# Performance work log

Measured on AMD Instinct MI355X. Metric: run time of the kernel, lower is better.

## Reference

```python
import jax, jax.numpy as jnp
import numpy as np
from jax import lax


def setup_inputs() -> dict:
    key = jax.random.key(0)
    k1, k2 = jax.random.split(key)
    B, T, C = 8, 4096, 256
    UNITS, WINDOW = 256, 2
    x = jax.random.normal(k1, (B, T, C), dtype=jnp.float32)
    kernel = jax.random.normal(k2, (WINDOW, C, 3 * UNITS), dtype=jnp.float32) * 0.05
    bias = jnp.zeros((3 * UNITS,), dtype=jnp.float32)
    return {"x": x, "kernel": kernel, "bias": bias}


def _qrnn_forward(x, kernel, bias):
    # Causal conv1d: left-pad time axis by (window - 1).
    window = kernel.shape[0]
    xp = jnp.pad(x, ((0, 0), (window - 1, 0), (0, 0)))
    gates = lax.conv_general_dilated(
        xp, kernel, window_strides=(1,), padding='VALID',
        dimension_numbers=('NWC', 'WIO', 'NWC')) + bias
    z, f, o = jnp.split(gates, 3, axis=-1)  # each [B, T, units]
    z = jnp.tanh(z)
    f = jax.nn.sigmoid(f)

    # fo_pool: c_t = f_t * c_{t-1} + (1 - f_t) * z_t, c_0 = 0.
    # Linear recurrence -> associative scan over time with elements (a, b):
    # compose((a1,b1),(a2,b2)) = (a1*a2, a2*b1 + b2).
    def combine(e1, e2):
        a1, b1 = e1
        a2, b2 = e2
        return a1 * a2, a2 * b1 + b2

    _, c = lax.associative_scan(combine, (f, (1.0 - f) * z), axis=1)
    h = jax.nn.sigmoid(o) * c  # output gate
    return h  # return_sequences=True -> [B, T, units]


def reference(x, kernel, bias):
    return _qrnn_forward(x, kernel, bias)
```

## Files before the change

### kernel.cpp

```cpp
#include <hip/hip_runtime.h>
#include <math.h>


#define Bq 8
#define Tq 4096
#define NCq 64
#define Lq 64

typedef __attribute__((ext_vector_type(8))) _Float16 f16x8;
typedef __attribute__((ext_vector_type(4))) float f32x4;

__device__ __forceinline__ float sigmoidf_(float x) {
    return 1.f / (1.f + __expf(-x));
}
__device__ __forceinline__ float tanh_fast(float x) {
    return 1.f - 2.f / (__expf(2.f * x) + 1.f);
}
__device__ __forceinline__ unsigned short f16b(float a) {
    _Float16 h = (_Float16)a;
    return *(unsigned short*)&h;
}
__device__ __forceinline__ void gload16(const void* g, void* l) {
    __builtin_amdgcn_global_load_lds(
        (const __attribute__((address_space(1))) void*)g,
        (__attribute__((address_space(3))) void*)l, 16, 0, 0);
}

__global__ __launch_bounds__(256) void split_x(
    const float* __restrict__ x, _Float16* __restrict__ xh)
{
    int idx = blockIdx.x * 256 + threadIdx.x;
    if (idx >= Bq * 4097 * 64) return;
    int b  = idx / (4097 * 64);
    int r  = idx % (4097 * 64);
    int tp = r / 64, c4 = (r % 64) << 2;
    size_t o = ((size_t)(b * 4097 + tp) << 8) + c4;
    _Float16 h4[4] = {(_Float16)0.f, (_Float16)0.f, (_Float16)0.f, (_Float16)0.f};
    if (tp > 0) {
        const float4 v = *(const float4*)&x[((size_t)(b * 4096 + tp - 1) << 8) + c4];
        h4[0] = (_Float16)v.x; h4[1] = (_Float16)v.y;
        h4[2] = (_Float16)v.z; h4[3] = (_Float16)v.w;
    }
    *(ushort4*)&xh[o] = *(ushort4*)h4;
}

__global__ __launch_bounds__(256) void split_k(
    const float* __restrict__ kw, _Float16* __restrict__ bh)
{
    int idx = blockIdx.x * 256 + threadIdx.x;
    if (idx >= 768 * 512) return;
    int n = idx >> 9, k = idx & 511;
    bh[((size_t)n << 9) + k] = (_Float16)kw[(size_t)k * 768 + n];
}

__global__ __launch_bounds__(256) void conv_gemm(
    const _Float16* __restrict__ xh, const _Float16* __restrict__ bth,
    const float* __restrict__ bias,
    _Float16* __restrict__ Z, _Float16* __restrict__ G, _Float16* __restrict__ SO)
{
    __shared__ __align__(16) char smem[32768];
    const int tid = threadIdx.x;
    const int l = tid & 63, w = tid >> 6;
    const int wr = w >> 1, wc = w & 1;
    const int bm = blockIdx.x;
    const int b  = bm >> 5;
    const int t0 = (bm & 31) << 7;
    const int n0 = blockIdx.y << 7;

    f32x4 acc[4][4] = {};

    const int rowT   = tid >> 2;
    const int slotSw = (tid & 3) ^ ((rowT >> 1) & 3);
    size_t gaBase = ((size_t)(b * 4097 + t0 + rowT) << 8) + (slotSw << 3);
    const int ldsW = w << 9;

    int offA[4];
    const int colB = (l >> 4) << 4;
    #pragma unroll
    for (int i = 0; i < 4; ++i) {
        int ra = wr * 64 + i * 16 + (l & 15);
        offA[i] = ((ra << 6) + colB) ^ (((ra >> 1) & 3) << 4);
    }
    size_t bB[4];
    #pragma unroll
    for (int ni = 0; ni < 4; ++ni)
        bB[ni] = ((size_t)(n0 + wc * 64 + ni * 16 + (l & 15)) << 9) + ((l >> 4) << 3);

    auto stageA = [&](int buf, int kk) {
        size_t ga = gaBase + (size_t)kk * 32;
        _Float16* pA = (_Float16*)smem + buf * 4096 + ldsW;
        gload16(xh + ga,         pA);
        gload16(xh + ga + 16384, pA + 2048);
    };
    auto loadB = [&](int kk, f16x8* fb) {
        #pragma unroll
        for (int ni = 0; ni < 4; ++ni)
            fb[ni] = *(const f16x8*)(bth + bB[ni] + (size_t)kk * 32);
    };
    auto computeA = [&](int buf, const f16x8* fb) {
        const char* bA = (const char*)smem + buf * 8192;
        f16x8 fa[4];
        #pragma unroll
        for (int i = 0; i < 4; ++i)
            fa[i] = *(const f16x8*)(bA + offA[i]);
        #pragma unroll
        for (int mi = 0; mi < 4; ++mi)
            #pragma unroll
            for (int ni = 0; ni < 4; ++ni)
                acc[mi][ni] = __builtin_amdgcn_mfma_f32_16x16x32_f16(
                    fa[mi], fb[ni], acc[mi][ni], 0, 0, 0);
    };

    f16x8 fbA[4], fbB[4];
    stageA(0, 0);
    loadB(0, fbA);
    __syncthreads();
    #pragma unroll
    for (int kp = 0; kp < 8; ++kp) {
        const int k0 = kp * 2;
        if (k0 + 1 < 16) { stageA(1, k0 + 1); loadB(k0 + 1, fbB); }
        computeA(0, fbA);
        if (k0 + 1 < 16) __syncthreads();
        if (k0 + 1 < 16) {
            if (k0 + 2 < 16) { stageA(0, k0 + 2); loadB(k0 + 2, fbA); }
            computeA(1, fbB);
            if (k0 + 2 < 16) __syncthreads();
        }
    }
    __syncthreads();

    const int gsel = (int)(blockIdx.y >> 1);
    float bb[4];
    #pragma unroll
    for (int ni = 0; ni < 4; ++ni)
        bb[ni] = bias[n0 + wc * 64 + ni * 16 + (l & 15)];

    unsigned short* Hd = (unsigned short*)smem;
    #pragma unroll
    for (int ni = 0; ni < 4; ++ni) {
        const int cl = wc * 64 + ni * 16 + (l & 15);
        #pragma unroll
        for (int mi = 0; mi < 4; ++mi)
            #pragma unroll
            for (int r = 0; r < 4; ++r) {
                const int trl = wr * 64 + mi * 16 + ((l >> 4) << 2) + r;
                float g = acc[mi][ni][r] + bb[ni];
                float a = (gsel == 0) ? tanh_fast(g)
                        : (gsel == 1) ? sigmoidf_(-g)
                                      : sigmoidf_(g);
                int byt = (trl << 8) + ((cl << 1) ^ (((trl >> 2) & 3) << 4));
                *(unsigned short*)((char*)Hd + byt) = f16b(a);
            }
    }
    __syncthreads();
    _Float16* Gg = (gsel == 0) ? Z : (gsel == 1) ? G : SO;
    const int u0 = n0 & 255;
    const size_t gbase = ((size_t)(b * 4096 + t0) << 8) + u0;
    #pragma unroll
    for (int j = 0; j < 8; ++j) {
        int hoff = tid * 8 + j * 2048;
        int row  = hoff >> 7;
        int cby  = (hoff & 127) << 1;
        int srcB = (row << 8) + (cby ^ (((row >> 2) & 3) << 4));
        int4 v = *(const int4*)((const char*)Hd + srcB);
        *(int4*)&Gg[gbase + ((size_t)row << 8) + (cby >> 1)] = v;
    }
}

__global__ __launch_bounds__(256) void chunk_reduce(
    const _Float16* __restrict__ Z, const _Float16* __restrict__ G,
    float* __restrict__ CA, float* __restrict__ CB)
{
    const int u = threadIdx.x;
    const int blk = blockIdx.x;
    const int b = blk >> 6, ck = blk & 63;
    size_t base = (((size_t)b << 12) + ck * Lq) * 256 + u;
    float A = 1.f, Bv = 0.f;
    #pragma unroll 8
    for (int s = 0; s < Lq; ++s) {
        size_t idx = base + (size_t)s * 256;
        float g = (float)G[idx];
        float z = (float)Z[idx];
        Bv = fmaf(1.f - g, Bv, g * z);
        A *= (1.f - g);
    }
    size_t cidx = ((size_t)b * NCq + ck) * 256 + u;
    CA[cidx] = A;
    CB[cidx] = Bv;
}

__global__ __launch_bounds__(256) void carry_scan(
    const float* __restrict__ CA, const float* __restrict__ CB,
    float* __restrict__ CIN)
{
    const int u = threadIdx.x;
    const int b = blockIdx.x;
    float c = 0.f;
    #pragma unroll 8
    for (int k = 0; k < NCq; ++k) {
        size_t idx = ((size_t)b * NCq + k) * 256 + u;
        CIN[idx] = c;
        c = fmaf(CA[idx], c, CB[idx]);
    }
}

__global__ __launch_bounds__(256) void apply_scan(
    const _Float16* __restrict__ Z, const _Float16* __restrict__ G,
    const _Float16* __restrict__ SO, const float* __restrict__ CIN,
    float* __restrict__ out)
{
    const int u = threadIdx.x;
    const int blk = blockIdx.x;
    const int b = blk >> 6, ck = blk & 63;
    float c = CIN[((size_t)b * NCq + ck) * 256 + u];
    size_t base = (((size_t)b << 12) + ck * Lq) * 256 + u;
    #pragma unroll 8
    for (int s = 0; s < Lq; ++s) {
        size_t idx = base + (size_t)s * 256;
        float g = (float)G[idx], z = (float)Z[idx];
        c = fmaf(1.f - g, c, g * z);
        out[idx] = (float)SO[idx] * c;
    }
}

extern "C" void kernel_launch(void* const* d_in, const int* in_sizes, int n_in,
                              void* d_out, int out_size, void* d_ws, size_t ws_size,
                              hipStream_t stream) {
    const float* x    = (const float*)d_in[0];
    const float* kw   = (const float*)d_in[1];
    const float* bias = (const float*)d_in[2];
    float* out = (float*)d_out;

    char* p = (char*)d_ws;
    _Float16* xh  = (_Float16*)p; p += (size_t)Bq * 4097 * 256 * 2;
    _Float16* bth = (_Float16*)p; p += (size_t)768 * 512 * 2;
    _Float16* Z   = (_Float16*)p; p += (size_t)Bq * Tq * 256 * 2;
    _Float16* G   = (_Float16*)p; p += (size_t)Bq * Tq * 256 * 2;
    _Float16* SO  = (_Float16*)p; p += (size_t)Bq * Tq * 256 * 2;
    float* CA  = (float*)p; p += (size_t)Bq * NCq * 256 * 4;
    float* CB  = (float*)p; p += (size_t)Bq * NCq * 256 * 4;
    float* CIN = (float*)p;

    split_x<<<(Bq * 4097 * 64 + 255) / 256, 256, 0, stream>>>(x, xh);
    split_k<<<(768 * 512 + 255) / 256, 256, 0, stream>>>(kw, bth);
    dim3 g1(256, 6);
    conv_gemm<<<g1, 256, 0, stream>>>(xh, bth, bias, Z, G, SO);
    chunk_reduce<<<512, 256, 0, stream>>>(Z, G, CA, CB);
    carry_scan<<<Bq, 256, 0, stream>>>(CA, CB, CIN);
    apply_scan<<<512, 256, 0, stream>>>(Z, G, SO, CIN, out);
}
```

Before: 106.2 us.

## Stage B tile through LDS with triple-buffered async loads and XCD-aware block remap

The conv GEMM now loads the weight tile into LDS with direct global-to-LDS loads, like the A tile, instead of having each wave read B fragments from global memory into registers. LDS grows to three 16KB stages, so loads run two k-steps ahead, gated by explicit vmcnt waits and raw barriers. The block index is also remapped so that consecutive blocks dispatched across the 8 XCDs share tiles for better L2 locality, and MFMA sections raise wave priority. The larger LDS footprint may lower occupancy, and the hand-tuned waitcnt values must match the number of loads issued per stage.

```diff
diff --git a/kernel.cpp b/kernel.cpp
--- a/kernel.cpp
+++ b/kernel.cpp
@@ -58,78 +58,85 @@
     const float* __restrict__ bias,
     _Float16* __restrict__ Z, _Float16* __restrict__ G, _Float16* __restrict__ SO)
 {
-    __shared__ __align__(16) char smem[32768];
+    __shared__ __align__(16) char smem[49152];
     const int tid = threadIdx.x;
     const int l = tid & 63, w = tid >> 6;
     const int wr = w >> 1, wc = w & 1;
-    const int bm = blockIdx.x;
+
+    const int p  = blockIdx.x + (blockIdx.y << 8);
+    const int Lw = (p & 7) * 192 + (p >> 3);
+    const int bm = Lw & 255;
+    const int by = Lw >> 8;
     const int b  = bm >> 5;
     const int t0 = (bm & 31) << 7;
-    const int n0 = blockIdx.y << 7;
+    const int n0 = by << 7;
 
     f32x4 acc[4][4] = {};
 
     const int rowT   = tid >> 2;
     const int slotSw = (tid & 3) ^ ((rowT >> 1) & 3);
     size_t gaBase = ((size_t)(b * 4097 + t0 + rowT) << 8) + (slotSw << 3);
+    size_t gbBase = ((size_t)(n0 + rowT) << 9) + (slotSw << 3);
     const int ldsW = w << 9;
 
-    int offA[4];
+    int offA[4], offB[4];
     const int colB = (l >> 4) << 4;
     #pragma unroll
     for (int i = 0; i < 4; ++i) {
         int ra = wr * 64 + i * 16 + (l & 15);
         offA[i] = ((ra << 6) + colB) ^ (((ra >> 1) & 3) << 4);
-    }
-    size_t bB[4];
-    #pragma unroll
-    for (int ni = 0; ni < 4; ++ni)
-        bB[ni] = ((size_t)(n0 + wc * 64 + ni * 16 + (l & 15)) << 9) + ((l >> 4) << 3);
-
-    auto stageA = [&](int buf, int kk) {
+        int rb = wc * 64 + i * 16 + (l & 15);
+        offB[i] = ((rb << 6) + colB) ^ (((rb >> 1) & 3) << 4);
+    }
+
+    auto stage = [&](int kk) {
+        const int buf = kk % 3;
+        _Float16* pA = (_Float16*)(smem + buf * 16384) + ldsW;
+        _Float16* pB = (_Float16*)(smem + buf * 16384 + 8192) + ldsW;
         size_t ga = gaBase + (size_t)kk * 32;
-        _Float16* pA = (_Float16*)smem + buf * 4096 + ldsW;
-        gload16(xh + ga,         pA);
-        gload16(xh + ga + 16384, pA + 2048);
+        size_t gb = gbBase + (size_t)kk * 32;
+        gload16(xh  + ga,          pA);
+        gload16(xh  + ga + 16384,  pA + 2048);
+        gload16(bth + gb,          pB);
+        gload16(bth + gb + 32768,  pB + 2048);
     };
-    auto loadB = [&](int kk, f16x8* fb) {
+
+    auto compute = [&](int kk) {
+        const char* bA = (const char*)smem + (kk % 3) * 16384;
+        const char* bB = bA + 8192;
+        f16x8 fa[4], fb[4];
         #pragma unroll
-        for (int ni = 0; ni < 4; ++ni)
-            fb[ni] = *(const f16x8*)(bth + bB[ni] + (size_t)kk * 32);
-    };
-    auto computeA = [&](int buf, const f16x8* fb) {
-        const char* bA = (const char*)smem + buf * 8192;
-        f16x8 fa[4];
-        #pragma unroll
-        for (int i = 0; i < 4; ++i)
+        for (int i = 0; i < 4; ++i) {
             fa[i] = *(const f16x8*)(bA + offA[i]);
+            fb[i] = *(const f16x8*)(bB + offB[i]);
+        }
+        __builtin_amdgcn_s_setprio(1);
         #pragma unroll
         for (int mi = 0; mi < 4; ++mi)
             #pragma unroll
             for (int ni = 0; ni < 4; ++ni)
                 acc[mi][ni] = __builtin_amdgcn_mfma_f32_16x16x32_f16(
                     fa[mi], fb[ni], acc[mi][ni], 0, 0, 0);
+        __builtin_amdgcn_s_setprio(0);
     };
 
-    f16x8 fbA[4], fbB[4];
-    stageA(0, 0);
-    loadB(0, fbA);
-    __syncthreads();
-    #pragma unroll
-    for (int kp = 0; kp < 8; ++kp) {
-        const int k0 = kp * 2;
-        if (k0 + 1 < 16) { stageA(1, k0 + 1); loadB(k0 + 1, fbB); }
-        computeA(0, fbA);
-        if (k0 + 1 < 16) __syncthreads();
-        if (k0 + 1 < 16) {
-            if (k0 + 2 < 16) { stageA(0, k0 + 2); loadB(k0 + 2, fbA); }
-            computeA(1, fbB);
-            if (k0 + 2 < 16) __syncthreads();
-        }
-    }
-    __syncthreads();
-
-    const int gsel = (int)(blockIdx.y >> 1);
+    stage(0);
+    stage(1);
+#define QSTEP(k, V) \
+    if ((k) + 2 < 16) stage((k) + 2); \
+    asm volatile("s_waitcnt vmcnt(" #V ")" ::: "memory"); \
+    __builtin_amdgcn_s_barrier(); \
+    compute(k); \
+    asm volatile("s_waitcnt lgkmcnt(0)" ::: "memory"); \
+    __builtin_amdgcn_sched_barrier(0); \
+    __builtin_amdgcn_s_barrier();
+    QSTEP(0, 8)  QSTEP(1, 8)  QSTEP(2, 8)  QSTEP(3, 8)
+    QSTEP(4, 8)  QSTEP(5, 8)  QSTEP(6, 8)  QSTEP(7, 8)
+    QSTEP(8, 8)  QSTEP(9, 8)  QSTEP(10, 8) QSTEP(11, 8)
+    QSTEP(12, 8) QSTEP(13, 8) QSTEP(14, 4) QSTEP(15, 0)
+#undef QSTEP
+
+    const int gsel = by >> 1;
     float bb[4];
     #pragma unroll
     for (int ni = 0; ni < 4; ++ni)
```

Measured after the change: 87.03 us. -18.0%, faster.

## Rewrite conv GEMM with 256x256 tiles, LDS-staged B, and explicit barrier pipeline

Applied to the files above, without the earlier changes.

The conv GEMM moves from 128x128 tiles with 4 waves to 256x256 tiles with 8 waves. Both A and B are now staged into a double-buffered 128KB LDS region through direct global-to-LDS loads with XOR swizzling. The K loop is fully unrolled into an explicit schedule that interleaves LDS fragment loads, async stages, raw s_barrier/vmcnt waits and setprio-raised MFMA bursts. The intent is more operand reuse and hiding of load latency behind MFMA. The cost is a large LDS footprint that limits occupancy, fewer blocks (384) for the machine, and higher register pressure from the 8x4 accumulator array.

```diff
diff --git a/kernel.cpp b/kernel.cpp
--- a/kernel.cpp
+++ b/kernel.cpp
@@ -53,116 +53,166 @@
     bh[((size_t)n << 9) + k] = (_Float16)kw[(size_t)k * 768 + n];
 }
 
-__global__ __launch_bounds__(256) void conv_gemm(
+__global__ __launch_bounds__(512, 2) void conv_gemm(
     const _Float16* __restrict__ xh, const _Float16* __restrict__ bth,
     const float* __restrict__ bias,
     _Float16* __restrict__ Z, _Float16* __restrict__ G, _Float16* __restrict__ SO)
 {
-    __shared__ __align__(16) char smem[32768];
+    __shared__ __align__(16) char smem[131072];
     const int tid = threadIdx.x;
     const int l = tid & 63, w = tid >> 6;
-    const int wr = w >> 1, wc = w & 1;
+    const int wrow = w >> 2, wcol = w & 3;
+    const int lg = l >> 4, l15 = l & 15;
+    const int sw7 = l15 & 7;
     const int bm = blockIdx.x;
-    const int b  = bm >> 5;
-    const int t0 = (bm & 31) << 7;
-    const int n0 = blockIdx.y << 7;
-
-    f32x4 acc[4][4] = {};
-
-    const int rowT   = tid >> 2;
-    const int slotSw = (tid & 3) ^ ((rowT >> 1) & 3);
-    size_t gaBase = ((size_t)(b * 4097 + t0 + rowT) << 8) + (slotSw << 3);
-    const int ldsW = w << 9;
-
-    int offA[4];
-    const int colB = (l >> 4) << 4;
-    #pragma unroll
-    for (int i = 0; i < 4; ++i) {
-        int ra = wr * 64 + i * 16 + (l & 15);
-        offA[i] = ((ra << 6) + colB) ^ (((ra >> 1) & 3) << 4);
-    }
-    size_t bB[4];
-    #pragma unroll
-    for (int ni = 0; ni < 4; ++ni)
-        bB[ni] = ((size_t)(n0 + wc * 64 + ni * 16 + (l & 15)) << 9) + ((l >> 4) << 3);
-
-    auto stageA = [&](int buf, int kk) {
-        size_t ga = gaBase + (size_t)kk * 32;
-        _Float16* pA = (_Float16*)smem + buf * 4096 + ldsW;
-        gload16(xh + ga,         pA);
-        gload16(xh + ga + 16384, pA + 2048);
-    };
-    auto loadB = [&](int kk, f16x8* fb) {
-        #pragma unroll
-        for (int ni = 0; ni < 4; ++ni)
-            fb[ni] = *(const f16x8*)(bth + bB[ni] + (size_t)kk * 32);
-    };
-    auto computeA = [&](int buf, const f16x8* fb) {
-        const char* bA = (const char*)smem + buf * 8192;
-        f16x8 fa[4];
-        #pragma unroll
-        for (int i = 0; i < 4; ++i)
-            fa[i] = *(const f16x8*)(bA + offA[i]);
+    const int by = blockIdx.y;
+    const int b  = bm >> 4;
+    const int t0 = (bm & 15) << 8;
+    const int n0 = by << 8;
+
+    f32x4 acc[8][4] = {};
+    f16x8 fa[4][2], fb[4][2];
+
+    const size_t aRowBase = (size_t)b * 4097 + t0;
+
+    auto stg = [&](int kt, int op, int half) {
+        char* base = smem + ((kt & 1) << 16) + (op << 15) + (half << 14) + tid * 16;
+        #pragma unroll
+        for (int j = 0; j < 2; ++j) {
+            int row = j * 64 + (tid >> 3);
+            int sw  = (tid & 7) ^ (row & 7);
+            const _Float16* g = (op == 0)
+              ? xh  + (aRowBase + half * 128 + row + (kt >> 2)) * 256 + ((kt & 3) << 6) + sw * 8
+              : bth + ((size_t)(n0 + half * 128 + row) << 9) + (kt << 6) + sw * 8;
+            gload16(g, base + j * 8192);
+        }
+    };
+
+    auto ldq0 = [&](int kt) {
+        const char* bA = smem + ((kt & 1) << 16) + (wrow << 14);
+        const char* bB = smem + ((kt & 1) << 16) + 32768 + ((wcol >> 1) << 14);
+        #pragma unroll
+        for (int mi = 0; mi < 4; ++mi) {
+            int ra = mi * 16 + l15;
+            #pragma unroll
+            for (int kh = 0; kh < 2; ++kh)
+                fa[mi][kh] = *(const f16x8*)(bA + (ra << 7) + ((((kh << 2) + lg) ^ sw7) << 4));
+        }
+        #pragma unroll
+        for (int ni = 0; ni < 2; ++ni) {
+            int rb = (wcol & 1) * 64 + ni * 16 + l15;
+            #pragma unroll
+            for (int kh = 0; kh < 2; ++kh)
+                fb[ni][kh] = *(const f16x8*)(bB + (rb << 7) + ((((kh << 2) + lg) ^ sw7) << 4));
+        }
+    };
+    auto ldq1 = [&](int kt) {
+        const char* bB = smem + ((kt & 1) << 16) + 32768 + ((wcol >> 1) << 14);
+        #pragma unroll
+        for (int ni = 2; ni < 4; ++ni) {
+            int rb = (wcol & 1) * 64 + ni * 16 + l15;
+            #pragma unroll
+            for (int kh = 0; kh < 2; ++kh)
+                fb[ni][kh] = *(const f16x8*)(bB + (rb << 7) + ((((kh << 2) + lg) ^ sw7) << 4));
+        }
+    };
+    auto ldq2 = [&](int kt) {
+        const char* bA = smem + ((kt & 1) << 16) + (wrow << 14);
+        #pragma unroll
+        for (int mi = 0; mi < 4; ++mi) {
+            int ra = (mi + 4) * 16 + l15;
+            #pragma unroll
+            for (int kh = 0; kh < 2; ++kh)
+                fa[mi][kh] = *(const f16x8*)(bA + (ra << 7) + ((((kh << 2) + lg) ^ sw7) << 4));
+        }
+    };
+    auto mmaq = [&](int am, int nb) {
+        __builtin_amdgcn_s_setprio(1);
         #pragma unroll
         for (int mi = 0; mi < 4; ++mi)
             #pragma unroll
-            for (int ni = 0; ni < 4; ++ni)
-                acc[mi][ni] = __builtin_amdgcn_mfma_f32_16x16x32_f16(
-                    fa[mi], fb[ni], acc[mi][ni], 0, 0, 0);
-    };
-
-    f16x8 fbA[4], fbB[4];
-    stageA(0, 0);
-    loadB(0, fbA);
-    __syncthreads();
-    #pragma unroll
-    for (int kp = 0; kp < 8; ++kp) {
-        const int k0 = kp * 2;
-        if (k0 + 1 < 16) { stageA(1, k0 + 1); loadB(k0 + 1, fbB); }
-        computeA(0, fbA);
-        if (k0 + 1 < 16) __syncthreads();
-        if (k0 + 1 < 16) {
-            if (k0 + 2 < 16) { stageA(0, k0 + 2); loadB(k0 + 2, fbA); }
-            computeA(1, fbB);
-            if (k0 + 2 < 16) __syncthreads();
-        }
-    }
-    __syncthreads();
-
-    const int gsel = (int)(blockIdx.y >> 1);
+            for (int nj = 0; nj < 2; ++nj)
+                #pragma unroll
+                for (int kh = 0; kh < 2; ++kh)
+                    acc[am + mi][nb + nj] = __builtin_amdgcn_mfma_f32_16x16x32_f16(
+                        fa[mi][kh], fb[nb + nj][kh], acc[am + mi][nb + nj], 0, 0, 0);
+        __builtin_amdgcn_s_setprio(0);
+    };
+
+#define BARM asm volatile("s_barrier" ::: "memory")
+#define VMW(N) asm volatile("s_waitcnt vmcnt(" #N ")" ::: "memory")
+
+    stg(0,1,0); stg(0,1,1); stg(0,0,0); stg(0,0,1); stg(1,1,0); stg(1,1,1);
+    VMW(4); BARM;
+
+    ldq0(0); stg(1,0,0);         BARM; mmaq(0,0); BARM;
+    ldq1(0); stg(1,0,1);         BARM; mmaq(0,2); BARM;
+    ldq2(0); stg(2,1,0);         BARM; mmaq(4,0); BARM;
+             stg(2,1,1); VMW(4); BARM; mmaq(4,2); BARM;
+    ldq0(1); stg(2,0,0);         BARM; mmaq(0,0); BARM;
+    ldq1(1); stg(2,0,1);         BARM; mmaq(0,2); BARM;
+    ldq2(1); stg(3,1,0);         BARM; mmaq(4,0); BARM;
+             stg(3,1,1); VMW(4); BARM; mmaq(4,2); BARM;
+    ldq0(2); stg(3,0,0);         BARM; mmaq(0,0); BARM;
+    ldq1(2); stg(3,0,1);         BARM; mmaq(0,2); BARM;
+    ldq2(2); stg(4,1,0);         BARM; mmaq(4,0); BARM;
+             stg(4,1,1); VMW(4); BARM; mmaq(4,2); BARM;
+    ldq0(3); stg(4,0,0);         BARM; mmaq(0,0); BARM;
+    ldq1(3); stg(4,0,1);         BARM; mmaq(0,2); BARM;
+    ldq2(3); stg(5,1,0);         BARM; mmaq(4,0); BARM;
+             stg(5,1,1); VMW(4); BARM; mmaq(4,2); BARM;
+    ldq0(4); stg(5,0,0);         BARM; mmaq(0,0); BARM;
+    ldq1(4); stg(5,0,1);         BARM; mmaq(0,2); BARM;
+    ldq2(4); stg(6,1,0);         BARM; mmaq(4,0); BARM;
+             stg(6,1,1); VMW(4); BARM; mmaq(4,2); BARM;
+    ldq0(5); stg(6,0,0);         BARM; mmaq(0,0); BARM;
+    ldq1(5); stg(6,0,1);         BARM; mmaq(0,2); BARM;
+    ldq2(5); stg(7,1,0);         BARM; mmaq(4,0); BARM;
+             stg(7,1,1); VMW(4); BARM; mmaq(4,2); BARM;
+    ldq0(6); stg(7,0,0);         BARM; mmaq(0,0); BARM;
+    ldq1(6); stg(7,0,1);         BARM; mmaq(0,2); BARM;
+    ldq2(6);                     BARM; mmaq(4,0); BARM;
+             VMW(0);             BARM; mmaq(4,2); BARM;
+    ldq0(7);                     BARM; mmaq(0,0); BARM;
+    ldq1(7);                     BARM; mmaq(0,2); BARM;
+    ldq2(7);                     BARM; mmaq(4,0); BARM;
+                                 BARM; mmaq(4,2); BARM;
+#undef BARM
+#undef VMW
+
+    const int gsel = by;
     float bb[4];
     #pragma unroll
     for (int ni = 0; ni < 4; ++ni)
-        bb[ni] = bias[n0 + wc * 64 + ni * 16 + (l & 15)];
+        bb[ni] = bias[(by << 8) + wcol * 64 + ni * 16 + l15];
 
     unsigned short* Hd = (unsigned short*)smem;
     #pragma unroll
     for (int ni = 0; ni < 4; ++ni) {
-        const int cl = wc * 64 + ni * 16 + (l & 15);
-        #pragma unroll
-        for (int mi = 0; mi < 4; ++mi)
+        const int cl = wcol * 64 + ni * 16 + l15;
+        #pragma unroll
+        for (int mi = 0; mi < 8; ++mi)
             #pragma unroll
             for (int r = 0; r < 4; ++r) {
-                const int trl = wr * 64 + mi * 16 + ((l >> 4) << 2) + r;
+                const int trl = wrow * 128 + mi * 16 + lg * 4 + r;
                 float g = acc[mi][ni][r] + bb[ni];
                 float a = (gsel == 0) ? tanh_fast(g)
                         : (gsel == 1) ? sigmoidf_(-g)
                                       : sigmoidf_(g);
-                int byt = (trl << 8) + ((cl << 1) ^ (((trl >> 2) & 3) << 4));
+                int byt = (trl << 9) + ((cl << 1) ^ (((trl >> 2) & 3) << 4));
                 *(unsigned short*)((char*)Hd + byt) = f16b(a);
             }
     }
     __syncthreads();
     _Float16* Gg = (gsel == 0) ? Z : (gsel == 1) ? G : SO;
-    const int u0 = n0 & 255;
-    const size_t gbase = ((size_t)(b * 4096 + t0) << 8) + u0;
+    const size_t gbase = ((size_t)(b * 4096 + t0)) << 8;
     #pragma unroll
-    for (int j = 0; j < 8; ++j) {
-        int hoff = tid * 8 + j * 2048;
-        int row  = hoff >> 7;
-        int cby  = (hoff & 127) << 1;
-        int srcB = (row << 8) + (cby ^ (((row >> 2) & 3) << 4));
-        int4 v = *(const int4*)((const char*)Hd + srcB);
+    for (int i = 0; i < 16; ++i) {
+        int off = (i * 512 + tid) << 4;
+        int row = off >> 9;
+        int cby = off & 511;
+        int src = (row << 9) + (cby ^ (((row >> 2) & 3) << 4));
+        int4 v = *(const int4*)((const char*)Hd + src);
         *(int4*)&Gg[gbase + ((size_t)row << 8) + (cby >> 1)] = v;
     }
 }
@@ -243,8 +293,8 @@
 
     split_x<<<(Bq * 4097 * 64 + 255) / 256, 256, 0, stream>>>(x, xh);
     split_k<<<(768 * 512 + 255) / 256, 256, 0, stream>>>(kw, bth);
-    dim3 g1(256, 6);
-    conv_gemm<<<g1, 256, 0, stream>>>(xh, bth, bias, Z, G, SO);
+    dim3 g1(128, 3);
+    conv_gemm<<<g1, 512, 0, stream>>>(xh, bth, bias, Z, G, SO);
     chunk_reduce<<<512, 256, 0, stream>>>(Z, G, CA, CB);
     carry_scan<<<Bq, 256, 0, stream>>>(CA, CB, CIN);
     apply_scan<<<512, 256, 0, stream>>>(Z, G, SO, CIN, out);
```

Measured after the change: 99.96 us. -5.9%, faster.
